# Performance work log

Hardware: AMD Instinct MI355X
Metric: run time of the kernel (lower is better)

## Reference

```python
import jax, jax.numpy as jnp
import numpy as np

B, D, H4, L, T, VOCAB, DMID = 256, 512, 2048, 3, 201, 128, 1024
START_IDX = 0


def setup_inputs() -> dict:
    key = jax.random.key(0)
    ks = jax.random.split(key, 8)
    s = lambda k, shape, scale=0.02: jax.random.normal(k, shape, jnp.float32) * scale
    return {
        "feat": jax.random.normal(ks[0], (B, D), jnp.float32),
        "Wvis": s(ks[1], (D, D)),
        "bvis": jnp.zeros((D,), jnp.float32),
        "embed": s(ks[2], (VOCAB, D)),
        "Wih": s(ks[3], (L, H4, D)),
        "Whh": s(ks[4], (L, H4, D)),
        "bih": jnp.zeros((L, H4), jnp.float32),
        "bhh": jnp.zeros((L, H4), jnp.float32),
        "W1": s(ks[5], (DMID, D)),
        "b1": jnp.zeros((DMID,), jnp.float32),
        "W2": s(ks[6], (VOCAB, DMID)),
        "b2": jnp.zeros((VOCAB,), jnp.float32),
    }


def reference(feat, Wvis, bvis, embed, Wih, Whh, bih, bhh, W1, b1, W2, b2):
    # visual_proj applied once in forward(), then again per-layer in _init_hidden
    feat_p = feat @ Wvis.T + bvis                    # [B,D]
    h0_layer = feat_p @ Wvis.T + bvis                # same for every layer
    h0 = jnp.tile(h0_layer[None], (L, 1, 1))         # [L,B,D]
    c0 = jnp.zeros_like(h0)
    inp0 = jnp.broadcast_to(embed[START_IDX], (B, D))  # embed(<sos>)

    def step(carry, _):
        inp, h, c = carry
        x = inp
        hs, cs = [], []
        for l in range(L):  # small fixed layer count
            g = x @ Wih[l].T + bih[l] + h[l] @ Whh[l].T + bhh[l]  # [B,4D]
            i, f, gg, o = jnp.split(g, 4, axis=-1)  # torch gate order i,f,g,o
            c_l = jax.nn.sigmoid(f) * c[l] + jax.nn.sigmoid(i) * jnp.tanh(gg)
            h_l = jax.nn.sigmoid(o) * jnp.tanh(c_l)
            hs.append(h_l)
            cs.append(c_l)
            x = h_l
        out = x  # top-layer output; dropout is identity in eval
        # inp = out.detach() in the original loop
        return (jax.lax.stop_gradient(out), jnp.stack(hs), jnp.stack(cs)), out

    _, outs = jax.lax.scan(step, (inp0, h0, c0), None, length=T)  # [T,B,D]
    res = outs.transpose(1, 0, 2)                                 # [B,T,D]
    mid = jax.nn.gelu(res @ W1.T + b1, approximate=False)         # torch GELU is erf-exact
    logits = mid @ W2.T + b2                                      # [B,T,V]
    return logits.transpose(0, 2, 1)                              # [B,V,T]
```

## Files before the change

### kernel.cpp

```cpp
#include <hip/hip_runtime.h>

#define NB   256
#define ND   512
#define NH4  2048
#define NL   3
#define NT   201
#define NV   128
#define NMID 1024

typedef _Float16 half8 __attribute__((ext_vector_type(8)));
typedef float f32x4 __attribute__((ext_vector_type(4)));

__device__ __forceinline__ float sigf(float x) { return 1.0f / (1.0f + __expf(-x)); }
__device__ __forceinline__ float tanh_(float x) {
  float e = __expf(-2.0f * fabsf(x));
  float t = (1.0f - e) / (1.0f + e);
  return x < 0.0f ? -t : t;
}

__device__ __forceinline__ half8 l2_load(const _Float16* p) {
  half8 v;
  asm volatile("global_load_dwordx4 %0, %1, off sc0" : "=v"(v) : "v"(p));
  return v;
}

__device__ __forceinline__ unsigned l2_rmw_add(unsigned* p, unsigned val) {
  unsigned v;
  asm volatile("global_atomic_add %0, %1, %2, off sc0\n\ts_waitcnt vmcnt(0)"
               : "=v"(v) : "v"(p), "v"(val) : "memory");
  return v;
}

__device__ __forceinline__ void xbar(unsigned* cnt, bool pref) {
  if (pref && threadIdx.x >= 256)
    asm volatile("s_waitcnt vmcnt(8)" ::: "memory");
  else
    asm volatile("s_waitcnt vmcnt(0)" ::: "memory");
  __syncthreads();
  if (threadIdx.x == 0) {
    unsigned old = l2_rmw_add(cnt, 1u);
    unsigned target = (old & ~31u) + 32u;
    int guard = 1 << 16;
    while (l2_rmw_add(cnt, 0u) < target && --guard)
      __builtin_amdgcn_s_sleep(2);
  }
  __syncthreads();
  asm volatile("buffer_inv" ::: "memory");
  __builtin_amdgcn_sched_barrier(0);
}

__global__ void prep_all(const float* __restrict__ Wih, const float* __restrict__ Whh,
                         const float* __restrict__ bih, const float* __restrict__ bhh,
                         const float* __restrict__ Wvis, const float* __restrict__ feat,
                         const float* __restrict__ embed, const float* __restrict__ W1,
                         const float* __restrict__ W2,
                         _Float16* __restrict__ Wp, float* __restrict__ bp,
                         _Float16* __restrict__ Wvis16, _Float16* __restrict__ feat16,
                         _Float16* __restrict__ x0, _Float16* __restrict__ W1h,
                         _Float16* __restrict__ W2h, unsigned* __restrict__ cnt) {
  size_t idx = (size_t)blockIdx.x * 256 + threadIdx.x;
  {
    int k = (int)(idx & 1023);
    int R = (int)((idx >> 10) & 2047);
    int l = (int)(idx >> 21);
    int dt = R >> 6, g = (R >> 4) & 3, di = R & 15;
    int col = g * 512 + dt * 16 + di;
    float v = (k < 512) ? Wih[((size_t)l * NH4 + col) * ND + k]
                        : Whh[((size_t)l * NH4 + col) * ND + (k - 512)];
    Wp[idx] = (_Float16)v;
  }
  if (idx < (size_t)NL * NH4) {
    int R = (int)(idx & 2047);
    int l = (int)(idx >> 11);
    int dt = R >> 6, g = (R >> 4) & 3, di = R & 15;
    int col = g * 512 + dt * 16 + di;
    bp[idx] = bih[l * NH4 + col] + bhh[l * NH4 + col];
  }
  if (idx < 512 * 512)  Wvis16[idx] = (_Float16)Wvis[idx];
  if (idx < 256 * 512)  feat16[idx] = (_Float16)feat[idx];
  if (idx < 256 * 512)  x0[idx]     = (_Float16)embed[idx & 511];
  if (idx < 1024 * 512) W1h[idx]    = (_Float16)W1[idx];
  if (idx < 128 * 1024) W2h[idx]    = (_Float16)W2[idx];
  if (idx < 1024) cnt[idx] = 0;
}

__global__ __launch_bounds__(512, 2) void lstm_persist(
    const _Float16* __restrict__ Wp,
    const float* __restrict__ bp,
    const _Float16* __restrict__ Wvis,
    const float* __restrict__ bvis,
    const _Float16* __restrict__ feat16,
    const _Float16* __restrict__ x0,
    _Float16* __restrict__ featp,
    _Float16* __restrict__ hbuf,
    _Float16* __restrict__ res,
    unsigned* __restrict__ cntbase) {
  __shared__ _Float16 wlds[64][1024];
  __shared__ float expart[4][32][16][4];

  const int tid = threadIdx.x;
  const int lane = tid & 63, w = tid >> 6;
  const int lr = lane & 15, lg = (lane >> 4) & 3;

  unsigned xcd;
  asm volatile("s_getreg_b32 %0, hwreg(HW_REG_XCC_ID)" : "=s"(xcd));
  xcd &= 7u;

  unsigned* rank_slot = (unsigned*)&expart[0][0][0][0];
  if (tid == 0)
    *rank_slot = __hip_atomic_fetch_add(cntbase + 256 + xcd * 32, 1u,
                                        __ATOMIC_RELAXED, __HIP_MEMORY_SCOPE_AGENT);
  __syncthreads();
  const int rank = (int)(*rank_slot & 31u);
  __syncthreads();

  const int dt = rank;
  const int m0 = (int)xcd * 32;
  const int d0 = rank * 16;
  unsigned* cnt = cntbase + xcd * 32;

  #pragma unroll 4
  for (int i = 0; i < 16; ++i) {
    int G = tid + 512 * i;
    int r = G >> 7, g = G & 127;
    *(half8*)&wlds[r][(g ^ (r & 7)) * 8] =
        *(const half8*)(Wp + ((size_t)(dt * 64 + r)) * 1024 + g * 8);
  }
  half8 wreg[2][4][4];
  #pragma unroll
  for (int ly = 0; ly < 2; ++ly)
    #pragma unroll
    for (int n = 0; n < 4; ++n)
      #pragma unroll
      for (int kk = 0; kk < 4; ++kk)
        wreg[ly][n][kk] = *(const half8*)(Wp +
          ((size_t)((ly + 1) * NH4 + dt * 64 + n * 16 + lr)) * 1024 + w * 128 + kk * 32 + lg * 8);

  const int di = tid & 15, cb = (tid >> 4) & 31;
  f32x4 breg4[3];
  #pragma unroll
  for (int l = 0; l < 3; ++l)
    #pragma unroll
    for (int g = 0; g < 4; ++g)
      breg4[l][g] = bp[l * NH4 + dt * 64 + g * 16 + di];

  {
    float* xb = &expart[0][0][0][0];
    const int wm2 = w & 1, wk = w >> 1;
    #pragma unroll 1
    for (int pg = 0; pg < 2; ++pg) {
      const _Float16* A = pg ? featp : feat16;
      half8 avp[4];
      #pragma unroll
      for (int kc = 0; kc < 4; ++kc)
        avp[kc] = l2_load(A + (size_t)(m0 + wm2 * 16 + lr) * ND + wk * 128 + kc * 32 + lg * 8);
      asm volatile("s_waitcnt vmcnt(0)" ::: "memory");
      __builtin_amdgcn_sched_barrier(0);
      f32x4 pacc = {0.f, 0.f, 0.f, 0.f};
      #pragma unroll
      for (int kc = 0; kc < 4; ++kc) {
        half8 bb = *(const half8*)(Wvis + (size_t)(d0 + lr) * ND + wk * 128 + kc * 32 + lg * 8);
        pacc = __builtin_amdgcn_mfma_f32_16x16x32_f16(avp[kc], bb, pacc, 0, 0, 0);
      }
      #pragma unroll
      for (int j = 0; j < 4; ++j)
        xb[wk * 512 + (wm2 * 16 + lg * 4 + j) * 16 + lr] = pacc[j];
      __syncthreads();
      {
        int m = tid >> 4, d = tid & 15;
        float v = xb[m * 16 + d] + xb[512 + m * 16 + d] + xb[1024 + m * 16 + d]
                + xb[1536 + m * 16 + d] + bvis[d0 + d];
        _Float16 hv = (_Float16)v;
        size_t off = (size_t)(m0 + m) * ND + d0 + d;
        if (pg == 0) featp[off] = hv;
        else {
          hbuf[(size_t)(0 * 2 + 1) * (NB * ND) + off] = hv;
          hbuf[(size_t)(1 * 2 + 1) * (NB * ND) + off] = hv;
          hbuf[(size_t)(2 * 2 + 1) * (NB * ND) + off] = hv;
        }
      }
      xbar(cnt, false);
    }
  }

  float cst[3] = {0.f, 0.f, 0.f};
  const size_t aoff0 = (size_t)(m0 + lr) * ND + (size_t)(w & 3) * 128 + lg * 8;
  const size_t aoff1 = aoff0 + (size_t)16 * ND;
  half8 av0[4], av1[4];

  #pragma unroll 1
  for (int t = 0; t < NT; ++t) {
    #pragma unroll
    for (int l = 0; l < 3; ++l) {
      const _Float16* xsrc = (l == 0)
        ? ((t == 0) ? x0 : hbuf + (size_t)(2 * 2 + ((t + 1) & 1)) * (NB * ND))
        : hbuf + (size_t)((l - 1) * 2 + (t & 1)) * (NB * ND);
      const _Float16* hsrc = hbuf + (size_t)(l * 2 + ((t + 1) & 1)) * (NB * ND);
      _Float16* hdst       = hbuf + (size_t)(l * 2 + (t & 1)) * (NB * ND);

      f32x4 acc[2][4];
      #pragma unroll
      for (int m = 0; m < 2; ++m)
        #pragma unroll
        for (int n = 0; n < 4; ++n)
          acc[m][n] = (f32x4){0.f, 0.f, 0.f, 0.f};

      if (w < 4) {
        #pragma unroll
        for (int kk = 0; kk < 4; ++kk) {
          av0[kk] = l2_load(xsrc + aoff0 + kk * 32);
          av1[kk] = l2_load(xsrc + aoff1 + kk * 32);
        }
        asm volatile("s_waitcnt vmcnt(4)"
                     : "+v"(av0[0]), "+v"(av0[1]), "+v"(av1[0]), "+v"(av1[1]));
        __builtin_amdgcn_s_setprio(1);
        #pragma unroll
        for (int kk = 0; kk < 2; ++kk)
          #pragma unroll
          for (int n = 0; n < 4; ++n) {
            half8 bf;
            if (l == 0) {
              int kg = w * 16 + kk * 4 + lg;
              bf = *(const half8*)&wlds[n * 16 + lr][(kg ^ (lr & 7)) * 8];
            } else bf = wreg[l - 1][n][kk];
            acc[0][n] = __builtin_amdgcn_mfma_f32_16x16x32_f16(av0[kk], bf, acc[0][n], 0, 0, 0);
            acc[1][n] = __builtin_amdgcn_mfma_f32_16x16x32_f16(av1[kk], bf, acc[1][n], 0, 0, 0);
          }
        __builtin_amdgcn_s_setprio(0);
        asm volatile("s_waitcnt vmcnt(0)"
                     : "+v"(av0[2]), "+v"(av0[3]), "+v"(av1[2]), "+v"(av1[3]));
        __builtin_amdgcn_s_setprio(1);
        #pragma unroll
        for (int kk = 2; kk < 4; ++kk)
          #pragma unroll
          for (int n = 0; n < 4; ++n) {
            half8 bf;
            if (l == 0) {
              int kg = w * 16 + kk * 4 + lg;
              bf = *(const half8*)&wlds[n * 16 + lr][(kg ^ (lr & 7)) * 8];
            } else bf = wreg[l - 1][n][kk];
            acc[0][n] = __builtin_amdgcn_mfma_f32_16x16x32_f16(av0[kk], bf, acc[0][n], 0, 0, 0);
            acc[1][n] = __builtin_amdgcn_mfma_f32_16x16x32_f16(av1[kk], bf, acc[1][n], 0, 0, 0);
          }
        __builtin_amdgcn_s_setprio(0);
      } else {
        if (t == 0 && l == 0) {
          #pragma unroll
          for (int kk = 0; kk < 4; ++kk) {
            av0[kk] = l2_load(hsrc + aoff0 + kk * 32);
            av1[kk] = l2_load(hsrc + aoff1 + kk * 32);
          }
        }
        asm volatile("s_waitcnt vmcnt(0)"
                     : "+v"(av0[0]), "+v"(av0[1]), "+v"(av0[2]), "+v"(av0[3]),
                       "+v"(av1[0]), "+v"(av1[1]), "+v"(av1[2]), "+v"(av1[3]));
        __builtin_amdgcn_s_setprio(1);
        #pragma unroll
        for (int kk = 0; kk < 4; ++kk)
          #pragma unroll
          for (int n = 0; n < 4; ++n) {
            half8 bf;
            if (l == 0) {
              int kg = w * 16 + kk * 4 + lg;
              bf = *(const half8*)&wlds[n * 16 + lr][(kg ^ (lr & 7)) * 8];
            } else bf = wreg[l - 1][n][kk];
            acc[0][n] = __builtin_amdgcn_mfma_f32_16x16x32_f16(av0[kk], bf, acc[0][n], 0, 0, 0);
            acc[1][n] = __builtin_amdgcn_mfma_f32_16x16x32_f16(av1[kk], bf, acc[1][n], 0, 0, 0);
          }
        __builtin_amdgcn_s_setprio(0);
      }

      if (w >= 4) {
        #pragma unroll
        for (int m = 0; m < 2; ++m)
          #pragma unroll
          for (int j = 0; j < 4; ++j) {
            f32x4 v = {acc[m][0][j], acc[m][1][j], acc[m][2][j], acc[m][3][j]};
            *(f32x4*)&expart[w - 4][m * 16 + lg * 4 + j][lr][0] = v;
          }
      }
      __syncthreads();
      if (w < 4) {
        #pragma unroll
        for (int m = 0; m < 2; ++m)
          #pragma unroll
          for (int j = 0; j < 4; ++j) {
            f32x4* pp = (f32x4*)&expart[w][m * 16 + lg * 4 + j][lr][0];
            f32x4 tv = *pp;
            tv[0] += acc[m][0][j]; tv[1] += acc[m][1][j];
            tv[2] += acc[m][2][j]; tv[3] += acc[m][3][j];
            *pp = tv;
          }
      }
      __syncthreads();

      {
        f32x4 s4 = breg4[l];
        #pragma unroll
        for (int s = 0; s < 4; ++s) {
          f32x4 g = *(const f32x4*)&expart[s][cb][di][0];
          s4 += g;
        }
        float c = cst[l];
        c = sigf(s4[1]) * c + sigf(s4[0]) * tanh_(s4[2]);
        cst[l] = c;
        _Float16 hv = (_Float16)(sigf(s4[3]) * tanh_(c));
        size_t off = (size_t)(m0 + cb) * ND + d0 + di;
        hdst[off] = hv;
        if (l == 2) res[(size_t)t * (NB * ND) + off] = hv;
      }

      if (!(t == NT - 1 && l == 2)) {
        if (w >= 4) {
          const int nt2 = (l == 2) ? t + 1 : t;
          const int nl  = (l == 2) ? 0 : l + 1;
          const _Float16* nh = hbuf + (size_t)(nl * 2 + ((nt2 + 1) & 1)) * (NB * ND);
          #pragma unroll
          for (int kk = 0; kk < 4; ++kk) {
            av0[kk] = l2_load(nh + aoff0 + kk * 32);
            av1[kk] = l2_load(nh + aoff1 + kk * 32);
          }
        }
        xbar(cnt, true);
      }
    }
  }
}

__global__ __launch_bounds__(256, 2) void head_kernel(
    const _Float16* __restrict__ res,
    const _Float16* __restrict__ W1h,
    const float* __restrict__ b1,
    const _Float16* __restrict__ W2h,
    const float* __restrict__ b2,
    float* __restrict__ out) {
  const int tid = threadIdx.x;
  const int lane = tid & 63, w = tid >> 6;
  const int lr = lane & 15, lg = (lane >> 4) & 3;
  const int r0 = blockIdx.x * 64;

  __shared__ _Float16 mid[4][64][128];

  f32x4 acc2[4][2];
  #pragma unroll
  for (int m = 0; m < 4; ++m)
    #pragma unroll
    for (int n2 = 0; n2 < 2; ++n2) acc2[m][n2] = (f32x4){0.f, 0.f, 0.f, 0.f};

  #pragma unroll 1
  for (int rr = 0; rr < 2; ++rr) {
    const int c = rr * 4 + w;
    #pragma unroll 1
    for (int nh = 0; nh < 2; ++nh) {
      f32x4 acc1[4][4];
      #pragma unroll
      for (int m = 0; m < 4; ++m)
        #pragma unroll
        for (int n = 0; n < 4; ++n) acc1[m][n] = (f32x4){0.f, 0.f, 0.f, 0.f};
      #pragma unroll 2
      for (int kc = 0; kc < 16; ++kc) {
        half8 af[4];
        #pragma unroll
        for (int m = 0; m < 4; ++m)
          af[m] = *(const half8*)(res + (size_t)(r0 + m * 16 + lr) * ND + kc * 32 + lg * 8);
        #pragma unroll
        for (int n = 0; n < 4; ++n) {
          half8 bb = *(const half8*)(W1h +
              (size_t)(c * 128 + nh * 64 + n * 16 + lr) * ND + kc * 32 + lg * 8);
          #pragma unroll
          for (int m = 0; m < 4; ++m)
            acc1[m][n] = __builtin_amdgcn_mfma_f32_16x16x32_f16(af[m], bb, acc1[m][n], 0, 0, 0);
        }
      }
      #pragma unroll
      for (int n = 0; n < 4; ++n)
        #pragma unroll
        for (int m = 0; m < 4; ++m)
          #pragma unroll
          for (int j = 0; j < 4; ++j) {
            int row = m * 16 + lg * 4 + j;
            int col = nh * 64 + n * 16 + lr;
            float v = acc1[m][n][j] + b1[c * 128 + col];
            v = 0.5f * v * (1.0f + erff(v * 0.7071067811865475f));
            int sw = (((col >> 3) ^ (row & 15)) << 3) + (col & 7);
            mid[w][row][sw] = (_Float16)v;
          }
    }
    __syncthreads();
    #pragma unroll 1
    for (int s = 0; s < 4; ++s) {
      #pragma unroll
      for (int kc2 = 0; kc2 < 4; ++kc2) {
        half8 a2[4];
        #pragma unroll
        for (int m = 0; m < 4; ++m) {
          int row = m * 16 + lr;
          int blk = (kc2 * 4 + lg) ^ (row & 15);
          a2[m] = *(const half8*)&mid[s][row][blk * 8];
        }
        #pragma unroll
        for (int n2 = 0; n2 < 2; ++n2) {
          half8 bb = *(const half8*)(W2h +
              (size_t)(w * 32 + n2 * 16 + lr) * NMID + rr * 512 + s * 128 + kc2 * 32 + lg * 8);
          #pragma unroll
          for (int m = 0; m < 4; ++m)
            acc2[m][n2] = __builtin_amdgcn_mfma_f32_16x16x32_f16(a2[m], bb, acc2[m][n2], 0, 0, 0);
        }
      }
    }
    __syncthreads();
  }
  #pragma unroll
  for (int n2 = 0; n2 < 2; ++n2)
    #pragma unroll
    for (int m = 0; m < 4; ++m)
      #pragma unroll
      for (int j = 0; j < 4; ++j) {
        int r = r0 + m * 16 + lg * 4 + j;
        int b = r & 255, t = r >> 8;
        int v = w * 32 + n2 * 16 + lr;
        out[((size_t)b * NV + v) * NT + t] = acc2[m][n2][j] + b2[v];
      }
}

extern "C" void kernel_launch(void* const* d_in, const int* in_sizes, int n_in,
                              void* d_out, int out_size, void* d_ws, size_t ws_size,
                              hipStream_t stream) {
  const float* feat  = (const float*)d_in[0];
  const float* Wvis  = (const float*)d_in[1];
  const float* bvis  = (const float*)d_in[2];
  const float* embed = (const float*)d_in[3];
  const float* Wih   = (const float*)d_in[4];
  const float* Whh   = (const float*)d_in[5];
  const float* bih   = (const float*)d_in[6];
  const float* bhh   = (const float*)d_in[7];
  const float* W1    = (const float*)d_in[8];
  const float* b1    = (const float*)d_in[9];
  const float* W2    = (const float*)d_in[10];
  const float* b2    = (const float*)d_in[11];
  float* out = (float*)d_out;

  char* p = (char*)d_ws;
  _Float16* Wp     = (_Float16*)p; p += (size_t)NL * NH4 * 1024 * 2;
  _Float16* Wvis16 = (_Float16*)p; p += (size_t)512 * 512 * 2;
  _Float16* feat16 = (_Float16*)p; p += (size_t)256 * 512 * 2;
  _Float16* x0     = (_Float16*)p; p += (size_t)256 * 512 * 2;
  _Float16* featp  = (_Float16*)p; p += (size_t)256 * 512 * 2;
  _Float16* hbuf   = (_Float16*)p; p += (size_t)NL * 2 * NB * ND * 2;
  _Float16* resb   = (_Float16*)p; p += (size_t)NT * NB * ND * 2;
  _Float16* W1h    = (_Float16*)p; p += (size_t)NMID * ND * 2;
  _Float16* W2h    = (_Float16*)p; p += (size_t)NV * NMID * 2;
  float*    bp     = (float*)p;    p += (size_t)NL * NH4 * 4;
  unsigned* cnt    = (unsigned*)p; p += 4096;

  prep_all<<<24576, 256, 0, stream>>>(Wih, Whh, bih, bhh, Wvis, feat, embed, W1, W2,
                                      Wp, bp, Wvis16, feat16, x0, W1h, W2h, cnt);
  lstm_persist<<<256, 512, 0, stream>>>(Wp, bp, Wvis16, bvis, feat16, x0,
                                        featp, hbuf, resb, cnt);
  head_kernel<<<804, 256, 0, stream>>>(resb, W1h, b1, W2h, b2, out);
  (void)in_sizes; (void)n_in; (void)out_size; (void)ws_size;
}
```

Baseline: 2.359 ms.

## Split grid barrier into arrive/wait and overlap next recurrent GEMM with wait

Splits the cross-block barrier into separate arrive and wait phases. Between them, the waves that handle the recurrent h@Whh part compute the next layer's partial product from already-prefetched hidden state and issue the prefetch for the following one, so that work overlaps the barrier spin. Launch bounds drop from 2 to 1 blocks per CU, giving more registers at the cost of occupancy. The prologue precomputes the first recurrent partial. The index bookkeeping for which hbuf slot to prefetch is delicate and could read stale data if it is wrong.

```diff
diff --git a/kernel.cpp b/kernel.cpp
--- a/kernel.cpp
+++ b/kernel.cpp
@@ -31,15 +31,18 @@
   return v;
 }
 
-__device__ __forceinline__ void xbar(unsigned* cnt, bool pref) {
-  if (pref && threadIdx.x >= 256)
-    asm volatile("s_waitcnt vmcnt(8)" ::: "memory");
-  else
-    asm volatile("s_waitcnt vmcnt(0)" ::: "memory");
+__device__ __forceinline__ unsigned bar_arrive(unsigned* cnt) {
+  asm volatile("s_waitcnt vmcnt(0)" ::: "memory");
   __syncthreads();
+  unsigned target = 0;
   if (threadIdx.x == 0) {
     unsigned old = l2_rmw_add(cnt, 1u);
-    unsigned target = (old & ~31u) + 32u;
+    target = (old & ~31u) + 32u;
+  }
+  return target;
+}
+__device__ __forceinline__ void bar_wait(unsigned* cnt, unsigned target) {
+  if (threadIdx.x == 0) {
     int guard = 1 << 16;
     while (l2_rmw_add(cnt, 0u) < target && --guard)
       __builtin_amdgcn_s_sleep(2);
@@ -84,7 +87,7 @@
   if (idx < 1024) cnt[idx] = 0;
 }
 
-__global__ __launch_bounds__(512, 2) void lstm_persist(
+__global__ __launch_bounds__(512, 1) void lstm_persist(
     const _Float16* __restrict__ Wp,
     const float* __restrict__ bp,
     const _Float16* __restrict__ Wvis,
@@ -179,33 +182,75 @@
           hbuf[(size_t)(2 * 2 + 1) * (NB * ND) + off] = hv;
         }
       }
-      xbar(cnt, false);
+      unsigned bt = bar_arrive(cnt);
+      bar_wait(cnt, bt);
     }
   }
 
-  float cst[3] = {0.f, 0.f, 0.f};
   const size_t aoff0 = (size_t)(m0 + lr) * ND + (size_t)(w & 3) * 128 + lg * 8;
   const size_t aoff1 = aoff0 + (size_t)16 * ND;
   half8 av0[4], av1[4];
 
+  if (w >= 4) {
+    const _Float16* h00 = hbuf + (size_t)(0 * 2 + 1) * (NB * ND);
+    #pragma unroll
+    for (int kk = 0; kk < 4; ++kk) {
+      av0[kk] = l2_load(h00 + aoff0 + kk * 32);
+      av1[kk] = l2_load(h00 + aoff1 + kk * 32);
+    }
+    asm volatile("s_waitcnt vmcnt(0)"
+                 : "+v"(av0[0]), "+v"(av0[1]), "+v"(av0[2]), "+v"(av0[3]),
+                   "+v"(av1[0]), "+v"(av1[1]), "+v"(av1[2]), "+v"(av1[3]));
+    f32x4 pacc[2][4];
+    #pragma unroll
+    for (int m = 0; m < 2; ++m)
+      #pragma unroll
+      for (int n = 0; n < 4; ++n) pacc[m][n] = (f32x4){0.f, 0.f, 0.f, 0.f};
+    #pragma unroll
+    for (int kk = 0; kk < 4; ++kk)
+      #pragma unroll
+      for (int n = 0; n < 4; ++n) {
+        int kg = w * 16 + kk * 4 + lg;
+        half8 bf = *(const half8*)&wlds[n * 16 + lr][(kg ^ (lr & 7)) * 8];
+        pacc[0][n] = __builtin_amdgcn_mfma_f32_16x16x32_f16(av0[kk], bf, pacc[0][n], 0, 0, 0);
+        pacc[1][n] = __builtin_amdgcn_mfma_f32_16x16x32_f16(av1[kk], bf, pacc[1][n], 0, 0, 0);
+      }
+    #pragma unroll
+    for (int m = 0; m < 2; ++m)
+      #pragma unroll
+      for (int j = 0; j < 4; ++j) {
+        f32x4 v = {pacc[m][0][j], pacc[m][1][j], pacc[m][2][j], pacc[m][3][j]};
+        *(f32x4*)&expart[w - 4][m * 16 + lg * 4 + j][lr][0] = v;
+      }
+    const _Float16* h11 = hbuf + (size_t)(1 * 2 + 1) * (NB * ND);
+    #pragma unroll
+    for (int kk = 0; kk < 4; ++kk) {
+      av0[kk] = l2_load(h11 + aoff0 + kk * 32);
+      av1[kk] = l2_load(h11 + aoff1 + kk * 32);
+    }
+  }
+  __syncthreads();
+
+  float cst[3] = {0.f, 0.f, 0.f};
+
   #pragma unroll 1
   for (int t = 0; t < NT; ++t) {
     #pragma unroll
     for (int l = 0; l < 3; ++l) {
+      const bool last = (t == NT - 1 && l == 2);
       const _Float16* xsrc = (l == 0)
         ? ((t == 0) ? x0 : hbuf + (size_t)(2 * 2 + ((t + 1) & 1)) * (NB * ND))
         : hbuf + (size_t)((l - 1) * 2 + (t & 1)) * (NB * ND);
-      const _Float16* hsrc = hbuf + (size_t)(l * 2 + ((t + 1) & 1)) * (NB * ND);
-      _Float16* hdst       = hbuf + (size_t)(l * 2 + (t & 1)) * (NB * ND);
+      _Float16* hdst = hbuf + (size_t)(l * 2 + (t & 1)) * (NB * ND);
 
       f32x4 acc[2][4];
-      #pragma unroll
-      for (int m = 0; m < 2; ++m)
-        #pragma unroll
-        for (int n = 0; n < 4; ++n)
-          acc[m][n] = (f32x4){0.f, 0.f, 0.f, 0.f};
 
       if (w < 4) {
+        #pragma unroll
+        for (int m = 0; m < 2; ++m)
+          #pragma unroll
+          for (int n = 0; n < 4; ++n)
+            acc[m][n] = (f32x4){0.f, 0.f, 0.f, 0.f};
         #pragma unroll
         for (int kk = 0; kk < 4; ++kk) {
           av0[kk] = l2_load(xsrc + aoff0 + kk * 32);
@@ -243,44 +288,7 @@
             acc[1][n] = __builtin_amdgcn_mfma_f32_16x16x32_f16(av1[kk], bf, acc[1][n], 0, 0, 0);
           }
         __builtin_amdgcn_s_setprio(0);
-      } else {
-        if (t == 0 && l == 0) {
-          #pragma unroll
-          for (int kk = 0; kk < 4; ++kk) {
-            av0[kk] = l2_load(hsrc + aoff0 + kk * 32);
-            av1[kk] = l2_load(hsrc + aoff1 + kk * 32);
-          }
-        }
-        asm volatile("s_waitcnt vmcnt(0)"
-                     : "+v"(av0[0]), "+v"(av0[1]), "+v"(av0[2]), "+v"(av0[3]),
-                       "+v"(av1[0]), "+v"(av1[1]), "+v"(av1[2]), "+v"(av1[3]));
-        __builtin_amdgcn_s_setprio(1);
-        #pragma unroll
-        for (int kk = 0; kk < 4; ++kk)
-          #pragma unroll
-          for (int n = 0; n < 4; ++n) {
-            half8 bf;
-            if (l == 0) {
-              int kg = w * 16 + kk * 4 + lg;
-              bf = *(const half8*)&wlds[n * 16 + lr][(kg ^ (lr & 7)) * 8];
-            } else bf = wreg[l - 1][n][kk];
-            acc[0][n] = __builtin_amdgcn_mfma_f32_16x16x32_f16(av0[kk], bf, acc[0][n], 0, 0, 0);
-            acc[1][n] = __builtin_amdgcn_mfma_f32_16x16x32_f16(av1[kk], bf, acc[1][n], 0, 0, 0);
-          }
-        __builtin_amdgcn_s_setprio(0);
-      }
-
-      if (w >= 4) {
-        #pragma unroll
-        for (int m = 0; m < 2; ++m)
-          #pragma unroll
-          for (int j = 0; j < 4; ++j) {
-            f32x4 v = {acc[m][0][j], acc[m][1][j], acc[m][2][j], acc[m][3][j]};
-            *(f32x4*)&expart[w - 4][m * 16 + lg * 4 + j][lr][0] = v;
-          }
-      }
-      __syncthreads();
-      if (w < 4) {
+
         #pragma unroll
         for (int m = 0; m < 2; ++m)
           #pragma unroll
@@ -310,18 +318,53 @@
         if (l == 2) res[(size_t)t * (NB * ND) + off] = hv;
       }
 
-      if (!(t == NT - 1 && l == 2)) {
+      if (!last) {
+        unsigned bt = bar_arrive(cnt);
+
         if (w >= 4) {
-          const int nt2 = (l == 2) ? t + 1 : t;
-          const int nl  = (l == 2) ? 0 : l + 1;
-          const _Float16* nh = hbuf + (size_t)(nl * 2 + ((nt2 + 1) & 1)) * (NB * ND);
-          #pragma unroll
-          for (int kk = 0; kk < 4; ++kk) {
-            av0[kk] = l2_load(nh + aoff0 + kk * 32);
-            av1[kk] = l2_load(nh + aoff1 + kk * 32);
+          asm volatile("s_waitcnt vmcnt(0)"
+                       : "+v"(av0[0]), "+v"(av0[1]), "+v"(av0[2]), "+v"(av0[3]),
+                         "+v"(av1[0]), "+v"(av1[1]), "+v"(av1[2]), "+v"(av1[3]));
+          #pragma unroll
+          for (int m = 0; m < 2; ++m)
+            #pragma unroll
+            for (int n = 0; n < 4; ++n)
+              acc[m][n] = (f32x4){0.f, 0.f, 0.f, 0.f};
+          __builtin_amdgcn_s_setprio(1);
+          #pragma unroll
+          for (int kk = 0; kk < 4; ++kk)
+            #pragma unroll
+            for (int n = 0; n < 4; ++n) {
+              half8 bf;
+              if (l == 2) {
+                int kg = w * 16 + kk * 4 + lg;
+                bf = *(const half8*)&wlds[n * 16 + lr][(kg ^ (lr & 7)) * 8];
+              } else bf = wreg[l][n][kk];
+              acc[0][n] = __builtin_amdgcn_mfma_f32_16x16x32_f16(av0[kk], bf, acc[0][n], 0, 0, 0);
+              acc[1][n] = __builtin_amdgcn_mfma_f32_16x16x32_f16(av1[kk], bf, acc[1][n], 0, 0, 0);
+            }
+          __builtin_amdgcn_s_setprio(0);
+          #pragma unroll
+          for (int m = 0; m < 2; ++m)
+            #pragma unroll
+            for (int j = 0; j < 4; ++j) {
+              f32x4 v = {acc[m][0][j], acc[m][1][j], acc[m][2][j], acc[m][3][j]};
+              *(f32x4*)&expart[w - 4][m * 16 + lg * 4 + j][lr][0] = v;
+            }
+          if (!(t == NT - 1 && l >= 1)) {
+            const _Float16* nh2 =
+              (l == 0) ? hbuf + (size_t)(4 + ((t + 1) & 1)) * (NB * ND) :
+              (l == 1) ? hbuf + (size_t)(0 + (t & 1)) * (NB * ND)
+                       : hbuf + (size_t)(2 + (t & 1)) * (NB * ND);
+            #pragma unroll
+            for (int kk = 0; kk < 4; ++kk) {
+              av0[kk] = l2_load(nh2 + aoff0 + kk * 32);
+              av1[kk] = l2_load(nh2 + aoff1 + kk * 32);
+            }
           }
         }
-        xbar(cnt, true);
+
+        bar_wait(cnt, bt);
       }
     }
   }
```

After: 2.468 ms (median of 2 runs). 4.6% more time.
